# Kernel tuning notes

Hardware: AMD Instinct MI355X
Metric: run time of the kernel (lower is better)

Reference implementation:

```python
import jax, jax.numpy as jnp
import numpy as np

VOCAB = 32000
EMB = 512       # embedding_size; also the sequence length per the source loop
HID = 512       # hidden_dim
NTAG = 36       # number of POS-tag-specific LSTMCells
OUT = 1         # output_size
SEQ = EMB       # forward iterates range(embedding_size)


def setup_inputs() -> dict:
    key = jax.random.key(0)
    ks = jax.random.split(key, 10)
    s = 1.0 / np.sqrt(HID)  # torch LSTMCell init: U(-1/sqrt(H), 1/sqrt(H))
    inp = {
        "x": jax.random.randint(ks[0], (1, SEQ), 0, VOCAB, dtype=jnp.int64)
             if jax.config.jax_enable_x64 else
             jax.random.randint(ks[0], (1, SEQ), 0, VOCAB, dtype=jnp.int32),
        "tag_ids": jax.random.randint(ks[1], (SEQ,), 0, NTAG, dtype=jnp.int32),
        "h0": jnp.zeros((1, HID), jnp.float32),
        "c0": jnp.zeros((1, HID), jnp.float32),
        # frozen pretrained embedding table
        "emb": jax.random.normal(ks[2], (VOCAB, EMB), jnp.float32) * 0.1,
        # stacked per-tag LSTMCell params, torch gate order (i, f, g, o)
        "W_ih": jax.random.uniform(ks[3], (NTAG, 4 * HID, EMB), jnp.float32, -s, s),
        "W_hh": jax.random.uniform(ks[4], (NTAG, 4 * HID, HID), jnp.float32, -s, s),
        "b_ih": jax.random.uniform(ks[5], (NTAG, 4 * HID), jnp.float32, -s, s),
        "b_hh": jax.random.uniform(ks[6], (NTAG, 4 * HID), jnp.float32, -s, s),
        "W_fc": jax.random.uniform(ks[7], (OUT, HID), jnp.float32, -s, s),
        "b_fc": jax.random.uniform(ks[8], (OUT,), jnp.float32, -s, s),
    }
    return inp


def _lstm_cell(x_t, h, c, Wih, Whh, bih, bhh):
    # x_t: [D], h/c: [H]; Wih: [4H, D], Whh: [4H, H]
    gates = Wih @ x_t + Whh @ h + bih + bhh      # [4H]
    i, f, g, o = jnp.split(gates, 4)
    i, f, o = jax.nn.sigmoid(i), jax.nn.sigmoid(f), jax.nn.sigmoid(o)
    g = jnp.tanh(g)
    c_new = f * c + i * g
    h_new = o * jnp.tanh(c_new)
    return h_new, c_new


def reference(x, tag_ids, h0, c0, emb, W_ih, W_hh, b_ih, b_hh, W_fc, b_fc):
    embeds = emb[x[0]]                            # [T, D] (batch is structurally 1)

    def step(carry, xs):
        h, c = carry
        x_t, tag = xs
        h, c = _lstm_cell(x_t, h, c, W_ih[tag], W_hh[tag], b_ih[tag], b_hh[tag])
        return (h, c), None

    (h, c), _ = jax.lax.scan(step, (h0[0], c0[0]), (embeds, tag_ids))
    # dropout is identity in eval; fc + sigmoid; out[:, -1]
    out = jax.nn.sigmoid(h @ W_fc.T + b_fc)       # [OUT]
    out = out.reshape(1, -1)[:, -1]               # [1]
    return out, h[None, :], c[None, :]
```

## Files before the change

### kernel.cpp

```cpp
#include <hip/hip_runtime.h>

#define VOCAB 32000
#define EMB 512
#define HID 512
#define NTAG 36
#define SEQ 512
#define G4H 2048
#define NBLK 128
#define XCHUNK 32

typedef unsigned long long ull;
typedef float f4 __attribute__((ext_vector_type(4)));

__device__ __forceinline__ float fast_tanh(float x) {
    float e = __expf(2.f * x);
    return 1.f - 2.f / (e + 1.f);
}
__device__ __forceinline__ float fast_sigmoid(float x) {
    return 1.f / (1.f + __expf(-x));
}

__global__ __launch_bounds__(256) void precompute_z(
    const int* __restrict__ x,
    const int* __restrict__ tag_ids,
    const float* __restrict__ emb,
    const float* __restrict__ W_ih,
    const float* __restrict__ b_ih,
    const float* __restrict__ b_hh,
    float* __restrict__ Z)
{
    __shared__ int list[SEQ];
    __shared__ int cnt;
    __shared__ __align__(16) float xc[XCHUNK][EMB];

    const int tid  = threadIdx.x;
    const int tag  = blockIdx.x;
    const int row0 = blockIdx.y * 64;
    const int wave = tid >> 6, lane = tid & 63;

    if (tid == 0) cnt = 0;
    __syncthreads();
    for (int t = tid; t < SEQ; t += 256)
        if (tag_ids[t] == tag) { int p = atomicAdd(&cnt, 1); list[p] = t; }
    __syncthreads();
    const int n = cnt;

    for (int c0 = 0; c0 < n; c0 += XCHUNK) {
        const int nc = min(XCHUNK, n - c0);
        __syncthreads();
        for (int idx = tid; idx < nc * 128; idx += 256) {
            int tl = idx >> 7, k4 = idx & 127;
            int t = list[c0 + tl];
            ((float4*)xc[tl])[k4] = ((const float4*)(emb + (size_t)x[t] * EMB))[k4];
        }
        __syncthreads();
        for (int rr = 0; rr < 16; rr += 4) {
            const int row = row0 + wave * 16 + rr;
            const float* w0p = W_ih + ((size_t)tag * G4H + row) * EMB;
            const float* w1p = w0p + EMB;
            const float* w2p = w0p + 2 * EMB;
            const float* w3p = w0p + 3 * EMB;
            const f4 wa0 = __builtin_nontemporal_load(&((const f4*)w0p)[lane]);
            const f4 wa1 = __builtin_nontemporal_load(&((const f4*)w0p)[64 + lane]);
            const f4 wb0 = __builtin_nontemporal_load(&((const f4*)w1p)[lane]);
            const f4 wb1 = __builtin_nontemporal_load(&((const f4*)w1p)[64 + lane]);
            const f4 wc0 = __builtin_nontemporal_load(&((const f4*)w2p)[lane]);
            const f4 wc1 = __builtin_nontemporal_load(&((const f4*)w2p)[64 + lane]);
            const f4 wd0 = __builtin_nontemporal_load(&((const f4*)w3p)[lane]);
            const f4 wd1 = __builtin_nontemporal_load(&((const f4*)w3p)[64 + lane]);
            const float bi0 = b_ih[tag * G4H + row]     + b_hh[tag * G4H + row];
            const float bi1 = b_ih[tag * G4H + row + 1] + b_hh[tag * G4H + row + 1];
            const float bi2 = b_ih[tag * G4H + row + 2] + b_hh[tag * G4H + row + 2];
            const float bi3 = b_ih[tag * G4H + row + 3] + b_hh[tag * G4H + row + 3];
            for (int tl = 0; tl < nc; ++tl) {
                float4 x0 = *(const float4*)&xc[tl][4 * lane];
                float4 x1 = *(const float4*)&xc[tl][256 + 4 * lane];
                float d0 = wa0.x*x0.x + wa0.y*x0.y + wa0.z*x0.z + wa0.w*x0.w
                         + wa1.x*x1.x + wa1.y*x1.y + wa1.z*x1.z + wa1.w*x1.w;
                float d1 = wb0.x*x0.x + wb0.y*x0.y + wb0.z*x0.z + wb0.w*x0.w
                         + wb1.x*x1.x + wb1.y*x1.y + wb1.z*x1.z + wb1.w*x1.w;
                float d2 = wc0.x*x0.x + wc0.y*x0.y + wc0.z*x0.z + wc0.w*x0.w
                         + wc1.x*x1.x + wc1.y*x1.y + wc1.z*x1.z + wc1.w*x1.w;
                float d3 = wd0.x*x0.x + wd0.y*x0.y + wd0.z*x0.z + wd0.w*x0.w
                         + wd1.x*x1.x + wd1.y*x1.y + wd1.z*x1.z + wd1.w*x1.w;
                #pragma unroll
                for (int m = 32; m >= 1; m >>= 1) {
                    d0 += __shfl_xor(d0, m, 64);
                    d1 += __shfl_xor(d1, m, 64);
                    d2 += __shfl_xor(d2, m, 64);
                    d3 += __shfl_xor(d3, m, 64);
                }
                if (lane == 0) {
                    float* zr = Z + (size_t)list[c0 + tl] * G4H + row;
                    zr[0] = d0 + bi0; zr[1] = d1 + bi1;
                    zr[2] = d2 + bi2; zr[3] = d3 + bi3;
                }
            }
        }
    }
}

__global__ __launch_bounds__(256) void lstm_seq(
    const int* __restrict__ tag_ids,
    const float* __restrict__ h0,
    const float* __restrict__ c0,
    const float* __restrict__ W_hh,
    const float* __restrict__ Z,
    const float* __restrict__ W_fc,
    const float* __restrict__ b_fc,
    ull* __restrict__ hist,
    float* __restrict__ d_out)
{
    __shared__ int tags[SEQ];
    __shared__ __align__(16) float hsh[2][HID];
    __shared__ float red[256];

    const int tid  = threadIdx.x;
    const int b    = blockIdx.x;
    const int wave = tid >> 6, lane = tid & 63;
    const int j    = b * 4 + wave;

    for (int t = tid; t < SEQ; t += 256) tags[t] = tag_ids[t];
    __syncthreads();

    float c    = (lane == 0) ? c0[j] : 0.f;
    float hval = 0.f;

    for (int t = 0; t < SEQ; ++t) {
        const int tag = tags[t];
        const float* wbase = W_hh + (size_t)tag * G4H * HID;
        const float4* r;
        r = (const float4*)(wbase + (size_t)(j)        * HID);
        float4 wi0 = r[lane], wi1 = r[64 + lane];
        r = (const float4*)(wbase + (size_t)(512 + j)  * HID);
        float4 wf0 = r[lane], wf1 = r[64 + lane];
        r = (const float4*)(wbase + (size_t)(1024 + j) * HID);
        float4 wg0 = r[lane], wg1 = r[64 + lane];
        r = (const float4*)(wbase + (size_t)(1536 + j) * HID);
        float4 wo0 = r[lane], wo1 = r[64 + lane];

        float zi = 0.f, zf = 0.f, zg = 0.f, zo = 0.f;
        if (lane == 0) {
            const float* zt = Z + (size_t)t * G4H;
            zi = zt[j]; zf = zt[512 + j]; zg = zt[1024 + j]; zo = zt[1536 + j];
        }

        asm volatile("s_waitcnt vmcnt(0)" ::: "memory");

        float v0, v1;
        if (t == 0) {
            v0 = h0[2 * tid]; v1 = h0[2 * tid + 1];
        } else {
            const ull* pa = hist + (size_t)(t - 1) * HID + 2 * tid;
            const ull* pb = pa + 1;
            const unsigned want = (unsigned)t;
            ull a0 = __hip_atomic_load(pa, __ATOMIC_RELAXED, __HIP_MEMORY_SCOPE_AGENT);
            ull b0 = __hip_atomic_load(pb, __ATOMIC_RELAXED, __HIP_MEMORY_SCOPE_AGENT);
            ull a1 = __hip_atomic_load(pa, __ATOMIC_RELAXED, __HIP_MEMORY_SCOPE_AGENT);
            ull b1 = __hip_atomic_load(pb, __ATOMIC_RELAXED, __HIP_MEMORY_SCOPE_AGENT);
            ull a2 = __hip_atomic_load(pa, __ATOMIC_RELAXED, __HIP_MEMORY_SCOPE_AGENT);
            ull b2 = __hip_atomic_load(pb, __ATOMIC_RELAXED, __HIP_MEMORY_SCOPE_AGENT);
            while ((unsigned)(a0 >> 32) != want || (unsigned)(b0 >> 32) != want) {
                a0 = a1; b0 = b1;
                a1 = a2; b1 = b2;
                a2 = __hip_atomic_load(pa, __ATOMIC_RELAXED, __HIP_MEMORY_SCOPE_AGENT);
                b2 = __hip_atomic_load(pb, __ATOMIC_RELAXED, __HIP_MEMORY_SCOPE_AGENT);
            }
            v0 = __uint_as_float((unsigned)a0);
            v1 = __uint_as_float((unsigned)b0);
        }
        const int hb = t & 1;
        hsh[hb][2 * tid]     = v0;
        hsh[hb][2 * tid + 1] = v1;
        __syncthreads();

        const float4 ha = *(const float4*)&hsh[hb][4 * lane];
        const float4 hc = *(const float4*)&hsh[hb][256 + 4 * lane];

        float di = wi0.x*ha.x + wi0.y*ha.y + wi0.z*ha.z + wi0.w*ha.w
                 + wi1.x*hc.x + wi1.y*hc.y + wi1.z*hc.z + wi1.w*hc.w;
        float df = wf0.x*ha.x + wf0.y*ha.y + wf0.z*ha.z + wf0.w*ha.w
                 + wf1.x*hc.x + wf1.y*hc.y + wf1.z*hc.z + wf1.w*hc.w;
        float dg = wg0.x*ha.x + wg0.y*ha.y + wg0.z*ha.z + wg0.w*ha.w
                 + wg1.x*hc.x + wg1.y*hc.y + wg1.z*hc.z + wg1.w*hc.w;
        float do_ = wo0.x*ha.x + wo0.y*ha.y + wo0.z*ha.z + wo0.w*ha.w
                  + wo1.x*hc.x + wo1.y*hc.y + wo1.z*hc.z + wo1.w*hc.w;
        #pragma unroll
        for (int m = 32; m >= 1; m >>= 1) {
            di  += __shfl_xor(di,  m, 64);
            df  += __shfl_xor(df,  m, 64);
            dg  += __shfl_xor(dg,  m, 64);
            do_ += __shfl_xor(do_, m, 64);
        }

        if (lane == 0) {
            float gi = zi + di, gf = zf + df, gg = zg + dg, go = zo + do_;
            float si = fast_sigmoid(gi);
            float sf = fast_sigmoid(gf);
            float so = fast_sigmoid(go);
            float tg = fast_tanh(gg);
            c = sf * c + si * tg;
            hval = so * fast_tanh(c);
            ull pk = ((ull)(unsigned)(t + 1) << 32) | (ull)__float_as_uint(hval);
            __hip_atomic_store(&hist[(size_t)t * HID + j], pk,
                               __ATOMIC_RELAXED, __HIP_MEMORY_SCOPE_AGENT);
        }
    }

    if (lane == 0) {
        d_out[1 + j]       = hval;
        d_out[1 + HID + j] = c;
    }

    if (b == 0) {
        const ull* hp = hist + (size_t)(SEQ - 1) * HID;
        ull a  = __hip_atomic_load(&hp[2 * tid],     __ATOMIC_RELAXED, __HIP_MEMORY_SCOPE_AGENT);
        ull bq = __hip_atomic_load(&hp[2 * tid + 1], __ATOMIC_RELAXED, __HIP_MEMORY_SCOPE_AGENT);
        while ((unsigned)(a >> 32) != (unsigned)SEQ || (unsigned)(bq >> 32) != (unsigned)SEQ) {
            a  = __hip_atomic_load(&hp[2 * tid],     __ATOMIC_RELAXED, __HIP_MEMORY_SCOPE_AGENT);
            bq = __hip_atomic_load(&hp[2 * tid + 1], __ATOMIC_RELAXED, __HIP_MEMORY_SCOPE_AGENT);
        }
        float s = __uint_as_float((unsigned)a)  * W_fc[2 * tid]
                + __uint_as_float((unsigned)bq) * W_fc[2 * tid + 1];
        red[tid] = s;
        __syncthreads();
        #pragma unroll
        for (int off = 128; off > 0; off >>= 1) {
            if (tid < off) red[tid] += red[tid + off];
            __syncthreads();
        }
        if (tid == 0)
            d_out[0] = fast_sigmoid(red[0] + b_fc[0]);
    }
}

extern "C" void kernel_launch(void* const* d_in, const int* in_sizes, int n_in,
                              void* d_out, int out_size, void* d_ws, size_t ws_size,
                              hipStream_t stream) {
    const int*   x       = (const int*)d_in[0];
    const int*   tag_ids = (const int*)d_in[1];
    const float* h0      = (const float*)d_in[2];
    const float* c0      = (const float*)d_in[3];
    const float* emb     = (const float*)d_in[4];
    const float* W_ih    = (const float*)d_in[5];
    const float* W_hh    = (const float*)d_in[6];
    const float* b_ih    = (const float*)d_in[7];
    const float* b_hh    = (const float*)d_in[8];
    const float* W_fc    = (const float*)d_in[9];
    const float* b_fc    = (const float*)d_in[10];
    float* out = (float*)d_out;

    const size_t zBytes = (size_t)SEQ * G4H * sizeof(float);
    float* Z    = (float*)d_ws;
    ull*   hist = (ull*)((char*)d_ws + zBytes);

    dim3 gA(NTAG, 32);
    precompute_z<<<gA, 256, 0, stream>>>(x, tag_ids, emb, W_ih, b_ih, b_hh, Z);
    lstm_seq<<<NBLK, 256, 0, stream>>>(tag_ids, h0, c0, W_hh, Z, W_fc, b_fc,
                                       hist, out);
}
```

Baseline: 1.340 ms.

## Warp-specialize LSTM recurrence with producer waves prefetching W_hh into LDS

```diff
diff --git a/kernel.cpp b/kernel.cpp
--- a/kernel.cpp
+++ b/kernel.cpp
@@ -100,7 +100,7 @@
     }
 }
 
-__global__ __launch_bounds__(256) void lstm_seq(
+__global__ __launch_bounds__(512) void lstm_seq(
     const int* __restrict__ tag_ids,
     const float* __restrict__ h0,
     const float* __restrict__ c0,
@@ -113,119 +113,186 @@
 {
     __shared__ int tags[SEQ];
     __shared__ __align__(16) float hsh[2][HID];
-    __shared__ float red[256];
+    __shared__ __align__(16) float wbuf[2][16][512];
+    __shared__ float zbuf[2][4][4];
 
     const int tid  = threadIdx.x;
     const int b    = blockIdx.x;
     const int wave = tid >> 6, lane = tid & 63;
-    const int j    = b * 4 + wave;
-
-    for (int t = tid; t < SEQ; t += 256) tags[t] = tag_ids[t];
+
+    for (int t = tid; t < SEQ; t += 512) tags[t] = tag_ids[t];
     __syncthreads();
 
-    float c    = (lane == 0) ? c0[j] : 0.f;
-    float hval = 0.f;
-
-    for (int t = 0; t < SEQ; ++t) {
-        const int tag = tags[t];
-        const float* wbase = W_hh + (size_t)tag * G4H * HID;
-        const float4* r;
-        r = (const float4*)(wbase + (size_t)(j)        * HID);
-        float4 wi0 = r[lane], wi1 = r[64 + lane];
-        r = (const float4*)(wbase + (size_t)(512 + j)  * HID);
-        float4 wf0 = r[lane], wf1 = r[64 + lane];
-        r = (const float4*)(wbase + (size_t)(1024 + j) * HID);
-        float4 wg0 = r[lane], wg1 = r[64 + lane];
-        r = (const float4*)(wbase + (size_t)(1536 + j) * HID);
-        float4 wo0 = r[lane], wo1 = r[64 + lane];
-
-        float zi = 0.f, zf = 0.f, zg = 0.f, zo = 0.f;
+    if (wave >= 4) {
+        const int wl = wave - 4;
+        const int jl = b * 4 + wl;
+
+        float4 A0, A1, A2, A3, A4, A5, A6, A7;
+        float4 B0, B1, B2, B3, B4, B5, B6, B7;
+        float  zA = 0.f, zB = 0.f;
+
+#define LISSUE(TT, R0,R1,R2,R3,R4,R5,R6,R7, ZR)                               \
+        do {                                                                   \
+            const int tg_ = tags[(TT)];                                        \
+            const float* wb_ = W_hh + (size_t)tg_ * (size_t)G4H * HID;         \
+            const float4* r_;                                                  \
+            r_ = (const float4*)(wb_ + (size_t)(jl)        * HID);             \
+            R0 = r_[lane]; R1 = r_[64 + lane];                                 \
+            r_ = (const float4*)(wb_ + (size_t)(512 + jl)  * HID);             \
+            R2 = r_[lane]; R3 = r_[64 + lane];                                 \
+            r_ = (const float4*)(wb_ + (size_t)(1024 + jl) * HID);             \
+            R4 = r_[lane]; R5 = r_[64 + lane];                                 \
+            r_ = (const float4*)(wb_ + (size_t)(1536 + jl) * HID);             \
+            R6 = r_[lane]; R7 = r_[64 + lane];                                 \
+            ZR = Z[(size_t)(TT) * G4H + 512 * (lane & 3) + jl];                \
+            asm volatile("" ::: "memory");                                     \
+        } while (0)
+
+#define LWRITE(SL, R0,R1,R2,R3,R4,R5,R6,R7, ZR)                               \
+        do {                                                                   \
+            float4* w_;                                                        \
+            w_ = (float4*)&wbuf[(SL)][wl * 4 + 0][0];                          \
+            w_[lane] = R0; w_[64 + lane] = R1;                                 \
+            w_ = (float4*)&wbuf[(SL)][wl * 4 + 1][0];                          \
+            w_[lane] = R2; w_[64 + lane] = R3;                                 \
+            w_ = (float4*)&wbuf[(SL)][wl * 4 + 2][0];                          \
+            w_[lane] = R4; w_[64 + lane] = R5;                                 \
+            w_ = (float4*)&wbuf[(SL)][wl * 4 + 3][0];                          \
+            w_[lane] = R6; w_[64 + lane] = R7;                                 \
+            if (lane < 4) zbuf[(SL)][wl][lane] = ZR;                           \
+        } while (0)
+
+        LISSUE(0, A0,A1,A2,A3,A4,A5,A6,A7, zA);
+        LISSUE(1, B0,B1,B2,B3,B4,B5,B6,B7, zB);
+        LWRITE(0, A0,A1,A2,A3,A4,A5,A6,A7, zA);
+        asm volatile("s_waitcnt lgkmcnt(0)" ::: "memory");
+        __builtin_amdgcn_sched_barrier(0);
+
+        for (int t = 0; t < SEQ; t += 2) {
+            __builtin_amdgcn_s_barrier();
+            if (t + 2 < SEQ) LISSUE(t + 2, A0,A1,A2,A3,A4,A5,A6,A7, zA);
+            LWRITE(1, B0,B1,B2,B3,B4,B5,B6,B7, zB);
+            asm volatile("s_waitcnt lgkmcnt(0)" ::: "memory");
+            __builtin_amdgcn_sched_barrier(0);
+            __builtin_amdgcn_s_barrier();
+            if (t + 3 < SEQ) LISSUE(t + 3, B0,B1,B2,B3,B4,B5,B6,B7, zB);
+            if (t + 2 < SEQ) {
+                LWRITE(0, A0,A1,A2,A3,A4,A5,A6,A7, zA);
+            }
+            asm volatile("s_waitcnt lgkmcnt(0)" ::: "memory");
+            __builtin_amdgcn_sched_barrier(0);
+        }
+#undef LISSUE
+#undef LWRITE
+    } else {
+        const int jc = b * 4 + wave;
+
+        float c    = (lane == 0) ? c0[jc] : 0.f;
+        float hval = 0.f;
+
+        for (int t = 0; t < SEQ; ++t) {
+            float v0, v1;
+            if (t == 0) {
+                v0 = h0[2 * tid]; v1 = h0[2 * tid + 1];
+            } else {
+                const ull* pa = hist + (size_t)(t - 1) * HID + 2 * tid;
+                const ull* pb = pa + 1;
+                const unsigned want = (unsigned)t;
+                ull a0 = __hip_atomic_load(pa, __ATOMIC_RELAXED, __HIP_MEMORY_SCOPE_AGENT);
+                ull b0 = __hip_atomic_load(pb, __ATOMIC_RELAXED, __HIP_MEMORY_SCOPE_AGENT);
+                ull a1 = __hip_atomic_load(pa, __ATOMIC_RELAXED, __HIP_MEMORY_SCOPE_AGENT);
+                ull b1 = __hip_atomic_load(pb, __ATOMIC_RELAXED, __HIP_MEMORY_SCOPE_AGENT);
+                ull a2 = __hip_atomic_load(pa, __ATOMIC_RELAXED, __HIP_MEMORY_SCOPE_AGENT);
+                ull b2 = __hip_atomic_load(pb, __ATOMIC_RELAXED, __HIP_MEMORY_SCOPE_AGENT);
+                while ((unsigned)(a0 >> 32) != want || (unsigned)(b0 >> 32) != want) {
+                    a0 = a1; b0 = b1;
+                    a1 = a2; b1 = b2;
+                    a2 = __hip_atomic_load(pa, __ATOMIC_RELAXED, __HIP_MEMORY_SCOPE_AGENT);
+                    b2 = __hip_atomic_load(pb, __ATOMIC_RELAXED, __HIP_MEMORY_SCOPE_AGENT);
+                }
+                v0 = __uint_as_float((unsigned)a0);
+                v1 = __uint_as_float((unsigned)b0);
+            }
+            const int hb = t & 1;
+            hsh[hb][2 * tid]     = v0;
+            hsh[hb][2 * tid + 1] = v1;
+            asm volatile("s_waitcnt lgkmcnt(0)" ::: "memory");
+            __builtin_amdgcn_sched_barrier(0);
+            __builtin_amdgcn_s_barrier();
+
+            const float4* r;
+            r = (const float4*)&wbuf[hb][wave * 4 + 0][0];
+            float4 wi0 = r[lane], wi1 = r[64 + lane];
+            r = (const float4*)&wbuf[hb][wave * 4 + 1][0];
+            float4 wf0 = r[lane], wf1 = r[64 + lane];
+            r = (const float4*)&wbuf[hb][wave * 4 + 2][0];
+            float4 wg0 = r[lane], wg1 = r[64 + lane];
+            r = (const float4*)&wbuf[hb][wave * 4 + 3][0];
+            float4 wo0 = r[lane], wo1 = r[64 + lane];
+
+            float zi = 0.f, zf = 0.f, zg = 0.f, zo = 0.f;
+            if (lane == 0) {
+                zi = zbuf[hb][wave][0]; zf = zbuf[hb][wave][1];
+                zg = zbuf[hb][wave][2]; zo = zbuf[hb][wave][3];
+            }
+
+            const float4 ha = *(const float4*)&hsh[hb][4 * lane];
+            const float4 hc = *(const float4*)&hsh[hb][256 + 4 * lane];
+
+            float di = wi0.x*ha.x + wi0.y*ha.y + wi0.z*ha.z + wi0.w*ha.w
+                     + wi1.x*hc.x + wi1.y*hc.y + wi1.z*hc.z + wi1.w*hc.w;
+            float df = wf0.x*ha.x + wf0.y*ha.y + wf0.z*ha.z + wf0.w*ha.w
+                     + wf1.x*hc.x + wf1.y*hc.y + wf1.z*hc.z + wf1.w*hc.w;
+            float dg = wg0.x*ha.x + wg0.y*ha.y + wg0.z*ha.z + wg0.w*ha.w
+                     + wg1.x*hc.x + wg1.y*hc.y + wg1.z*hc.z + wg1.w*hc.w;
+            float do_ = wo0.x*ha.x + wo0.y*ha.y + wo0.z*ha.z + wo0.w*ha.w
+                      + wo1.x*hc.x + wo1.y*hc.y + wo1.z*hc.z + wo1.w*hc.w;
+            #pragma unroll
+            for (int m = 32; m >= 1; m >>= 1) {
+                di  += __shfl_xor(di,  m, 64);
+                df  += __shfl_xor(df,  m, 64);
+                dg  += __shfl_xor(dg,  m, 64);
+                do_ += __shfl_xor(do_, m, 64);
+            }
+
+            if (lane == 0) {
+                float gi = zi + di, gf = zf + df, gg = zg + dg, go = zo + do_;
+                float si = fast_sigmoid(gi);
+                float sf = fast_sigmoid(gf);
+                float so = fast_sigmoid(go);
+                float tg = fast_tanh(gg);
+                c = sf * c + si * tg;
+                hval = so * fast_tanh(c);
+                ull pk = ((ull)(unsigned)(t + 1) << 32) | (ull)__float_as_uint(hval);
+                __hip_atomic_store(&hist[(size_t)t * HID + jc], pk,
+                                   __ATOMIC_RELAXED, __HIP_MEMORY_SCOPE_AGENT);
+            }
+        }
+
         if (lane == 0) {
-            const float* zt = Z + (size_t)t * G4H;
-            zi = zt[j]; zf = zt[512 + j]; zg = zt[1024 + j]; zo = zt[1536 + j];
-        }
-
-        asm volatile("s_waitcnt vmcnt(0)" ::: "memory");
-
-        float v0, v1;
-        if (t == 0) {
-            v0 = h0[2 * tid]; v1 = h0[2 * tid + 1];
-        } else {
-            const ull* pa = hist + (size_t)(t - 1) * HID + 2 * tid;
-            const ull* pb = pa + 1;
-            const unsigned want = (unsigned)t;
-            ull a0 = __hip_atomic_load(pa, __ATOMIC_RELAXED, __HIP_MEMORY_SCOPE_AGENT);
-            ull b0 = __hip_atomic_load(pb, __ATOMIC_RELAXED, __HIP_MEMORY_SCOPE_AGENT);
-            ull a1 = __hip_atomic_load(pa, __ATOMIC_RELAXED, __HIP_MEMORY_SCOPE_AGENT);
-            ull b1 = __hip_atomic_load(pb, __ATOMIC_RELAXED, __HIP_MEMORY_SCOPE_AGENT);
-            ull a2 = __hip_atomic_load(pa, __ATOMIC_RELAXED, __HIP_MEMORY_SCOPE_AGENT);
-            ull b2 = __hip_atomic_load(pb, __ATOMIC_RELAXED, __HIP_MEMORY_SCOPE_AGENT);
-            while ((unsigned)(a0 >> 32) != want || (unsigned)(b0 >> 32) != want) {
-                a0 = a1; b0 = b1;
-                a1 = a2; b1 = b2;
-                a2 = __hip_atomic_load(pa, __ATOMIC_RELAXED, __HIP_MEMORY_SCOPE_AGENT);
-                b2 = __hip_atomic_load(pb, __ATOMIC_RELAXED, __HIP_MEMORY_SCOPE_AGENT);
-            }
-            v0 = __uint_as_float((unsigned)a0);
-            v1 = __uint_as_float((unsigned)b0);
-        }
-        const int hb = t & 1;
-        hsh[hb][2 * tid]     = v0;
-        hsh[hb][2 * tid + 1] = v1;
-        __syncthreads();
-
-        const float4 ha = *(const float4*)&hsh[hb][4 * lane];
-        const float4 hc = *(const float4*)&hsh[hb][256 + 4 * lane];
-
-        float di = wi0.x*ha.x + wi0.y*ha.y + wi0.z*ha.z + wi0.w*ha.w
-                 + wi1.x*hc.x + wi1.y*hc.y + wi1.z*hc.z + wi1.w*hc.w;
-        float df = wf0.x*ha.x + wf0.y*ha.y + wf0.z*ha.z + wf0.w*ha.w
-                 + wf1.x*hc.x + wf1.y*hc.y + wf1.z*hc.z + wf1.w*hc.w;
-        float dg = wg0.x*ha.x + wg0.y*ha.y + wg0.z*ha.z + wg0.w*ha.w
-                 + wg1.x*hc.x + wg1.y*hc.y + wg1.z*hc.z + wg1.w*hc.w;
-        float do_ = wo0.x*ha.x + wo0.y*ha.y + wo0.z*ha.z + wo0.w*ha.w
-                  + wo1.x*hc.x + wo1.y*hc.y + wo1.z*hc.z + wo1.w*hc.w;
-        #pragma unroll
-        for (int m = 32; m >= 1; m >>= 1) {
-            di  += __shfl_xor(di,  m, 64);
-            df  += __shfl_xor(df,  m, 64);
-            dg  += __shfl_xor(dg,  m, 64);
-            do_ += __shfl_xor(do_, m, 64);
-        }
-
-        if (lane == 0) {
-            float gi = zi + di, gf = zf + df, gg = zg + dg, go = zo + do_;
-            float si = fast_sigmoid(gi);
-            float sf = fast_sigmoid(gf);
-            float so = fast_sigmoid(go);
-            float tg = fast_tanh(gg);
-            c = sf * c + si * tg;
-            hval = so * fast_tanh(c);
-            ull pk = ((ull)(unsigned)(t + 1) << 32) | (ull)__float_as_uint(hval);
-            __hip_atomic_store(&hist[(size_t)t * HID + j], pk,
-                               __ATOMIC_RELAXED, __HIP_MEMORY_SCOPE_AGENT);
+            d_out[1 + jc]       = hval;
+            d_out[1 + HID + jc] = c;
         }
     }
 
-    if (lane == 0) {
-        d_out[1 + j]       = hval;
-        d_out[1 + HID + j] = c;
-    }
-
     if (b == 0) {
-        const ull* hp = hist + (size_t)(SEQ - 1) * HID;
-        ull a  = __hip_atomic_load(&hp[2 * tid],     __ATOMIC_RELAXED, __HIP_MEMORY_SCOPE_AGENT);
-        ull bq = __hip_atomic_load(&hp[2 * tid + 1], __ATOMIC_RELAXED, __HIP_MEMORY_SCOPE_AGENT);
-        while ((unsigned)(a >> 32) != (unsigned)SEQ || (unsigned)(bq >> 32) != (unsigned)SEQ) {
-            a  = __hip_atomic_load(&hp[2 * tid],     __ATOMIC_RELAXED, __HIP_MEMORY_SCOPE_AGENT);
-            bq = __hip_atomic_load(&hp[2 * tid + 1], __ATOMIC_RELAXED, __HIP_MEMORY_SCOPE_AGENT);
-        }
-        float s = __uint_as_float((unsigned)a)  * W_fc[2 * tid]
-                + __uint_as_float((unsigned)bq) * W_fc[2 * tid + 1];
+        float* red = &hsh[0][0];
+        float s = 0.f;
+        if (tid < 256) {
+            const ull* hp = hist + (size_t)(SEQ - 1) * HID;
+            ull a  = __hip_atomic_load(&hp[2 * tid],     __ATOMIC_RELAXED, __HIP_MEMORY_SCOPE_AGENT);
+            ull bq = __hip_atomic_load(&hp[2 * tid + 1], __ATOMIC_RELAXED, __HIP_MEMORY_SCOPE_AGENT);
+            while ((unsigned)(a >> 32) != (unsigned)SEQ || (unsigned)(bq >> 32) != (unsigned)SEQ) {
+                a  = __hip_atomic_load(&hp[2 * tid],     __ATOMIC_RELAXED, __HIP_MEMORY_SCOPE_AGENT);
+                bq = __hip_atomic_load(&hp[2 * tid + 1], __ATOMIC_RELAXED, __HIP_MEMORY_SCOPE_AGENT);
+            }
+            s = __uint_as_float((unsigned)a)  * W_fc[2 * tid]
+              + __uint_as_float((unsigned)bq) * W_fc[2 * tid + 1];
+        }
         red[tid] = s;
         __syncthreads();
         #pragma unroll
-        for (int off = 128; off > 0; off >>= 1) {
+        for (int off = 256; off > 0; off >>= 1) {
             if (tid < off) red[tid] += red[tid + off];
             __syncthreads();
         }
@@ -256,6 +323,6 @@
 
     dim3 gA(NTAG, 32);
     precompute_z<<<gA, 256, 0, stream>>>(x, tag_ids, emb, W_ih, b_ih, b_hh, Z);
-    lstm_seq<<<NBLK, 256, 0, stream>>>(tag_ids, h0, c0, W_hh, Z, W_fc, b_fc,
+    lstm_seq<<<NBLK, 512, 0, stream>>>(tag_ids, h0, c0, W_hh, Z, W_fc, b_fc,
                                        hist, out);
 }
```

After: 2.451 ms. 82.9% more time.
